# Performance work log

Hardware: AMD Instinct MI355X
Metric: run time of the kernel (lower is better)

Reference implementation:

```python
import jax, jax.numpy as jnp
import numpy as np

H = 32          # query heads
HKV = 8         # kv heads
HD = 128        # head dim
BS = 64         # sparse block size
LOCAL = 16      # local blocks
VERT = 8        # vertical stride
STEP = 1        # head sliding step = max(1, VERT // H) for non-homo heads
BASE = 1000000.0
ROPE_SCALE = 1.0
SCALE = 1.0 / np.sqrt(HD)


def setup_inputs() -> dict:
    key = jax.random.key(0)
    ks = jax.random.split(key, 6)
    T, D = 2048, H * HD
    std = 0.02
    return {
        'hidden_states': jax.random.normal(ks[0], (T, D), jnp.float32),
        'positions': jnp.arange(T, dtype=jnp.int32),
        'Wq': jax.random.normal(ks[1], (D, H * HD), jnp.float32) * std,
        'bq': jnp.zeros((H * HD,), jnp.float32),
        'Wk': jax.random.normal(ks[2], (D, HKV * HD), jnp.float32) * std,
        'bk': jnp.zeros((HKV * HD,), jnp.float32),
        'Wv': jax.random.normal(ks[3], (D, HKV * HD), jnp.float32) * std,
        'bv': jnp.zeros((HKV * HD,), jnp.float32),
        'Wo': jax.random.normal(ks[4], (D, D), jnp.float32) * std,
        'bo': jnp.zeros((D,), jnp.float32),
    }


def _rope_cos_sin(positions):
    # neox-style rotary, linear scaling (factor 1.0 -> identity)
    inv_freq = 1.0 / (BASE ** (jnp.arange(0, HD, 2, dtype=jnp.float32) / HD))  # [HD/2]
    t = positions.astype(jnp.float32) / ROPE_SCALE                             # [T]
    freqs = t[:, None] * inv_freq[None, :]                                     # [T, HD/2]
    return jnp.cos(freqs), jnp.sin(freqs)


def _apply_rope(x, cos, sin):
    # x: [T, h, HD], neox: rotate halves
    x1, x2 = x[..., : HD // 2], x[..., HD // 2 :]
    c, s = cos[:, None, :], sin[:, None, :]
    return jnp.concatenate([x1 * c - x2 * s, x2 * c + x1 * s], axis=-1)


def _block_sparse_mask(T):
    # per-head local + vertical-stride block pattern, causal at token level
    blk = jnp.arange(T) // BS
    qb, kb = blk[:, None], blk[None, :]                      # [T,T] block ids
    heads = jnp.arange(H)
    local = (qb - kb) < LOCAL                                # [T,T]
    vert = ((kb[None, :, :] + heads[:, None, None] * STEP + 1) % VERT) == 0  # [H,T,T]
    causal = jnp.arange(T)[:, None] >= jnp.arange(T)[None, :]
    return causal[None] & (local[None] | vert)               # [H,T,T] bool


def reference(hidden_states, positions, Wq, bq, Wk, bk, Wv, bv, Wo, bo):
    T = hidden_states.shape[0]
    q = (hidden_states @ Wq + bq).reshape(T, H, HD)
    k = (hidden_states @ Wk + bk).reshape(T, HKV, HD)
    v = (hidden_states @ Wv + bv).reshape(T, HKV, HD)

    cos, sin = _rope_cos_sin(positions)
    q = _apply_rope(q, cos, sin)
    k = _apply_rope(k, cos, sin)

    # GQA: repeat kv heads to match query heads
    k = jnp.repeat(k, H // HKV, axis=1)   # [T,H,HD]
    v = jnp.repeat(v, H // HKV, axis=1)

    scores = jnp.einsum('shd,thd->hst', q, k) * SCALE         # [H,T,T]
    mask = _block_sparse_mask(T)
    scores = jnp.where(mask, scores, jnp.finfo(scores.dtype).min)
    probs = jax.nn.softmax(scores, axis=-1)
    out = jnp.einsum('hst,thd->shd', probs, v).reshape(T, H * HD)
    return out @ Wo + bo
```

## Files before the change

kernel.cpp:

```cpp
#include <hip/hip_runtime.h>
#include <type_traits>

#define H_    32
#define HKV_  8
#define HD_   128
#define D_    4096
#define KVD_  1024
#define NQKV_ 6144

typedef __attribute__((ext_vector_type(8))) short s8v;
typedef __attribute__((ext_vector_type(4))) float f4v;

__device__ __forceinline__ float b2f(unsigned short u) {
  union { unsigned int i; float f; } v; v.i = ((unsigned int)u) << 16; return v.f;
}
__device__ __forceinline__ unsigned short f2b(float f) {
  unsigned int u = __float_as_uint(f);
  u += 0x7fffu + ((u >> 16) & 1u);
  return (unsigned short)(u >> 16);
}

__device__ __forceinline__ void gload16(const unsigned short* g, unsigned short* l) {
  __builtin_amdgcn_global_load_lds((const __attribute__((address_space(1))) void*)g,
                                   (__attribute__((address_space(3))) void*)l, 16, 0, 0);
}

__global__ void cvt_bf16(const float* __restrict__ x, unsigned short* __restrict__ y,
                         int n8)
{
  int i = blockIdx.x * blockDim.x + threadIdx.x;
  if (i >= n8) return;
  const float4* xp = (const float4*)x + (size_t)i * 2;
  float4 a = xp[0], b = xp[1];
  s8v v;
  v[0] = (short)f2b(a.x); v[1] = (short)f2b(a.y);
  v[2] = (short)f2b(a.z); v[3] = (short)f2b(a.w);
  v[4] = (short)f2b(b.x); v[5] = (short)f2b(b.y);
  v[6] = (short)f2b(b.z); v[7] = (short)f2b(b.w);
  *(s8v*)(y + (size_t)i * 8) = v;
}

__global__ void concat_bias(const float* __restrict__ bq, const float* __restrict__ bk,
                            const float* __restrict__ bv, float* __restrict__ o)
{
  int i = blockIdx.x * blockDim.x + threadIdx.x;
  float v = (i < D_) ? bq[i] : (i < D_ + KVD_) ? bk[i - D_] : bv[i - D_ - KVD_];
  o[i] = v;
}

__global__ __launch_bounds__(256) void cvt_transpose(
    const float* __restrict__ W, unsigned short* __restrict__ Wt, int K, int N)
{
  __shared__ unsigned short tile[64][72];
  const int k0 = blockIdx.y * 64, n0 = blockIdx.x * 64;
  const int tid = threadIdx.x;
#pragma unroll
  for (int it = 0; it < 4; ++it) {
    int idx = tid + it * 256;
    int r = idx >> 4;
    int c = (idx & 15) << 2;
    float4 w = *(const float4*)(W + (size_t)(k0 + r) * N + n0 + c);
    tile[c + 0][r] = f2b(w.x); tile[c + 1][r] = f2b(w.y);
    tile[c + 2][r] = f2b(w.z); tile[c + 3][r] = f2b(w.w);
  }
  __syncthreads();
#pragma unroll
  for (int it = 0; it < 2; ++it) {
    int idx = tid + it * 256;
    int n = idx >> 3;
    int kk = (idx & 7) << 3;
    *(s8v*)(Wt + (size_t)(n0 + n) * K + k0 + kk) = *(const s8v*)&tile[n][kk];
  }
}

__global__ __launch_bounds__(256) void vtrans(
    const unsigned short* __restrict__ S, int lds_, unsigned short* __restrict__ Dst,
    int T)
{
  __shared__ unsigned short tile[64][72];
  const int v0 = blockIdx.x * 64, t0 = blockIdx.y * 64;
  const int tid = threadIdx.x;
#pragma unroll
  for (int it = 0; it < 2; ++it) {
    int idx = tid + it * 256;
    int tr = idx >> 3;
    int vc = (idx & 7) << 3;
    s8v val = *(const s8v*)(S + (size_t)(t0 + tr) * lds_ + v0 + vc);
#pragma unroll
    for (int u = 0; u < 8; ++u) tile[vc + u][tr] = (unsigned short)val[u];
  }
  __syncthreads();
#pragma unroll
  for (int it = 0; it < 2; ++it) {
    int idx = tid + it * 256;
    int vr = idx >> 3;
    int tc = (idx & 7) << 3;
    *(s8v*)(Dst + (size_t)(v0 + vr) * T + t0 + tc) = *(const s8v*)&tile[vr][tc];
  }
}

template <typename OT>
__global__ __launch_bounds__(512, 2) void gemm_bt4p(
    const unsigned short* __restrict__ A, const unsigned short* __restrict__ Bt,
    const float* __restrict__ bias, OT* __restrict__ C,
    int M, int N, int K, int ldc)
{
  __shared__ __align__(16) unsigned short lds[65536];

  const int tid  = threadIdx.x;
  const int wave = tid >> 6;
  const int lane = tid & 63;
  const int l16  = lane & 15;
  const int quad = lane >> 4;
  const int wm   = wave >> 2;
  const int wn   = wave & 3;

  const int nbx = N >> 8;
  const int nwg = nbx * (M >> 8);
  int bid = blockIdx.x;
  if ((nwg & 7) == 0) bid = (bid & 7) * (nwg >> 3) + (bid >> 3);
  const int row0 = (bid / nbx) << 8;
  const int col0 = (bid % nbx) << 8;

  const int srow = lane >> 2;
  const int scol = (((lane & 3) ^ ((lane >> 3) & 3)) << 3);
  const unsigned short* ApL = A  + (size_t)(row0 + wave * 32 + srow) * K + scol;
  const unsigned short* BpL = Bt + (size_t)(col0 + wave * 32 + srow) * K + scol;

  unsigned short* ldsA = lds;
  unsigned short* ldsB = lds + 32768;
  const int wst = wave * 1024;

  const int sl = ((quad ^ ((l16 >> 1) & 3)) << 3);
  const int arow = wm * 128 + l16;
  const int brow = wn * 64 + l16;

  f4v acc[8][4] = {};
  const int nt = K >> 6;

  {
    const unsigned short* sa = ApL;
    const unsigned short* sb = BpL;
    gload16(sa,                       ldsA + wst);
    gload16(sa + 16 * (size_t)K,      ldsA + wst + 512);
    gload16(sb,                       ldsB + wst);
    gload16(sb + 16 * (size_t)K,      ldsB + wst + 512);
    gload16(sa + 32,                  ldsA + 8192 + wst);
    gload16(sa + 32 + 16 * (size_t)K, ldsA + 8192 + wst + 512);
    gload16(sb + 32,                  ldsB + 8192 + wst);
    gload16(sb + 32 + 16 * (size_t)K, ldsB + 8192 + wst + 512);
  }
  asm volatile("s_waitcnt vmcnt(4)" ::: "memory");
  asm volatile("s_barrier" ::: "memory");

  for (int t = 0; t < nt; ++t) {
    const int p = t & 1;
    const unsigned short* Ab0 = ldsA + p * 16384;
    const unsigned short* Ab1 = Ab0 + 8192;
    const unsigned short* Bb0 = ldsB + p * 16384;
    const unsigned short* Bb1 = Bb0 + 8192;
    unsigned short* An = ldsA + (p ^ 1) * 16384;
    unsigned short* Bn = ldsB + (p ^ 1) * 16384;
    const bool pre = (t + 1 < nt);
    const unsigned short* sa = ApL + (size_t)(t + 1) * 64;
    const unsigned short* sb = BpL + (size_t)(t + 1) * 64;

    s8v a[8], b0, b1, b2, b3;

    b0 = *(const s8v*)&Bb0[(brow +  0) * 32 + sl];
    b1 = *(const s8v*)&Bb0[(brow + 16) * 32 + sl];
#pragma unroll
    for (int i = 0; i < 8; ++i)
      a[i] = *(const s8v*)&Ab0[(arow + i * 16) * 32 + sl];
    if (pre) {
      gload16(sa,                  An + wst);
      gload16(sa + 16 * (size_t)K, An + wst + 512);
    }
    __builtin_amdgcn_s_setprio(1);
#pragma unroll
    for (int i = 0; i < 8; ++i) {
      acc[i][0] = __builtin_amdgcn_mfma_f32_16x16x32_bf16(a[i], b0, acc[i][0], 0, 0, 0);
      acc[i][1] = __builtin_amdgcn_mfma_f32_16x16x32_bf16(a[i], b1, acc[i][1], 0, 0, 0);
    }
    __builtin_amdgcn_s_setprio(0);

    b2 = *(const s8v*)&Bb0[(brow + 32) * 32 + sl];
    b3 = *(const s8v*)&Bb0[(brow + 48) * 32 + sl];
    if (pre) {
      gload16(sb,                  Bn + wst);
      gload16(sb + 16 * (size_t)K, Bn + wst + 512);
      asm volatile("s_waitcnt vmcnt(4)" ::: "memory");
    } else {
      asm volatile("s_waitcnt vmcnt(0)" ::: "memory");
    }
    asm volatile("s_barrier" ::: "memory");
    __builtin_amdgcn_s_setprio(1);
#pragma unroll
    for (int i = 0; i < 8; ++i) {
      acc[i][2] = __builtin_amdgcn_mfma_f32_16x16x32_bf16(a[i], b2, acc[i][2], 0, 0, 0);
      acc[i][3] = __builtin_amdgcn_mfma_f32_16x16x32_bf16(a[i], b3, acc[i][3], 0, 0, 0);
    }
    __builtin_amdgcn_s_setprio(0);

    b2 = *(const s8v*)&Bb1[(brow + 32) * 32 + sl];
    b3 = *(const s8v*)&Bb1[(brow + 48) * 32 + sl];
#pragma unroll
    for (int i = 0; i < 8; ++i)
      a[i] = *(const s8v*)&Ab1[(arow + i * 16) * 32 + sl];
    if (pre) {
      gload16(sa + 32,                  An + 8192 + wst);
      gload16(sa + 32 + 16 * (size_t)K, An + 8192 + wst + 512);
    }
    __builtin_amdgcn_s_setprio(1);
#pragma unroll
    for (int i = 0; i < 8; ++i) {
      acc[i][2] = __builtin_amdgcn_mfma_f32_16x16x32_bf16(a[i], b2, acc[i][2], 0, 0, 0);
      acc[i][3] = __builtin_amdgcn_mfma_f32_16x16x32_bf16(a[i], b3, acc[i][3], 0, 0, 0);
    }
    __builtin_amdgcn_s_setprio(0);

    b0 = *(const s8v*)&Bb1[(brow +  0) * 32 + sl];
    b1 = *(const s8v*)&Bb1[(brow + 16) * 32 + sl];
    if (pre) {
      gload16(sb + 32,                  Bn + 8192 + wst);
      gload16(sb + 32 + 16 * (size_t)K, Bn + 8192 + wst + 512);
      asm volatile("s_waitcnt vmcnt(4)" ::: "memory");
    }
    asm volatile("s_barrier" ::: "memory");
    __builtin_amdgcn_s_setprio(1);
#pragma unroll
    for (int i = 0; i < 8; ++i) {
      acc[i][0] = __builtin_amdgcn_mfma_f32_16x16x32_bf16(a[i], b0, acc[i][0], 0, 0, 0);
      acc[i][1] = __builtin_amdgcn_mfma_f32_16x16x32_bf16(a[i], b1, acc[i][1], 0, 0, 0);
    }
    __builtin_amdgcn_s_setprio(0);
  }

#pragma unroll
  for (int j = 0; j < 4; ++j) {
    const int col = col0 + wn * 64 + j * 16 + l16;
    const float bc = bias[col];
#pragma unroll
    for (int i = 0; i < 8; ++i) {
      const int rowb = row0 + wm * 128 + i * 16 + quad * 4;
#pragma unroll
      for (int r = 0; r < 4; ++r) {
        float o = acc[i][j][r] + bc;
        if constexpr (std::is_same_v<OT, float>) C[(size_t)(rowb + r) * ldc + col] = o;
        else                                     C[(size_t)(rowb + r) * ldc + col] = f2b(o);
      }
    }
  }
}

__global__ __launch_bounds__(256, 2) void gemm_o128(
    const unsigned short* __restrict__ A, const unsigned short* __restrict__ Bt,
    const float* __restrict__ bias, float* __restrict__ C,
    int M, int N, int K)
{
  __shared__ __align__(16) unsigned short lds[32768];

  const int tid  = threadIdx.x;
  const int wave = tid >> 6;
  const int lane = tid & 63;
  const int l16  = lane & 15;
  const int quad = lane >> 4;
  const int wm   = wave >> 1;
  const int wn   = wave & 1;

  const int nbx = N >> 7;
  const int nwg = nbx * (M >> 7);
  int bid = blockIdx.x;
  if ((nwg & 7) == 0) bid = (bid & 7) * (nwg >> 3) + (bid >> 3);
  const int row0 = (bid / nbx) << 7;
  const int col0 = (bid % nbx) << 7;

  const int srow = lane >> 2;
  const int scol = (((lane & 3) ^ ((lane >> 3) & 3)) << 3);
  const unsigned short* ApL = A  + (size_t)(row0 + wave * 16 + srow) * K + scol;
  const unsigned short* BpL = Bt + (size_t)(col0 + wave * 16 + srow) * K + scol;

  unsigned short* ldsA = lds;
  unsigned short* ldsB = lds + 16384;
  const int wst = wave * 512;

  const int sl = ((quad ^ ((l16 >> 1) & 3)) << 3);
  const int arow = wm * 64 + l16;
  const int brow = wn * 64 + l16;

  f4v acc[4][4] = {};
  const int nt = K >> 6;

  {
    const unsigned short* sa = ApL;
    const unsigned short* sb = BpL;
    gload16(sa,                       ldsA + wst);
    gload16(sa + 64 * (size_t)K,      ldsA + wst + 2048);
    gload16(sb,                       ldsB + wst);
    gload16(sb + 64 * (size_t)K,      ldsB + wst + 2048);
    gload16(sa + 32,                  ldsA + 4096 + wst);
    gload16(sa + 32 + 64 * (size_t)K, ldsA + 4096 + wst + 2048);
    gload16(sb + 32,                  ldsB + 4096 + wst);
    gload16(sb + 32 + 64 * (size_t)K, ldsB + 4096 + wst + 2048);
  }
  asm volatile("s_waitcnt vmcnt(4)" ::: "memory");
  asm volatile("s_barrier" ::: "memory");

  for (int t = 0; t < nt; ++t) {
    const int p = t & 1;
    const unsigned short* Ab0 = ldsA + p * 8192;
    const unsigned short* Ab1 = Ab0 + 4096;
    const unsigned short* Bb0 = ldsB + p * 8192;
    const unsigned short* Bb1 = Bb0 + 4096;
    unsigned short* An = ldsA + (p ^ 1) * 8192;
    unsigned short* Bn = ldsB + (p ^ 1) * 8192;
    const bool pre = (t + 1 < nt);
    const unsigned short* sa = ApL + (size_t)(t + 1) * 64;
    const unsigned short* sb = BpL + (size_t)(t + 1) * 64;

    s8v a[4], b0, b1, b2, b3;

    b0 = *(const s8v*)&Bb0[(brow +  0) * 32 + sl];
    b1 = *(const s8v*)&Bb0[(brow + 16) * 32 + sl];
#pragma unroll
    for (int i = 0; i < 4; ++i)
      a[i] = *(const s8v*)&Ab0[(arow + i * 16) * 32 + sl];
    if (pre) {
      gload16(sa,                  An + wst);
      gload16(sa + 64 * (size_t)K, An + wst + 2048);
    }
    __builtin_amdgcn_s_setprio(1);
#pragma unroll
    for (int i = 0; i < 4; ++i) {
      acc[i][0] = __builtin_amdgcn_mfma_f32_16x16x32_bf16(a[i], b0, acc[i][0], 0, 0, 0);
      acc[i][1] = __builtin_amdgcn_mfma_f32_16x16x32_bf16(a[i], b1, acc[i][1], 0, 0, 0);
    }
    __builtin_amdgcn_s_setprio(0);

    b2 = *(const s8v*)&Bb0[(brow + 32) * 32 + sl];
    b3 = *(const s8v*)&Bb0[(brow + 48) * 32 + sl];
    if (pre) {
      gload16(sb,                  Bn + wst);
      gload16(sb + 64 * (size_t)K, Bn + wst + 2048);
      asm volatile("s_waitcnt vmcnt(4)" ::: "memory");
    } else {
      asm volatile("s_waitcnt vmcnt(0)" ::: "memory");
    }
    asm volatile("s_barrier" ::: "memory");
    __builtin_amdgcn_s_setprio(1);
#pragma unroll
    for (int i = 0; i < 4; ++i) {
      acc[i][2] = __builtin_amdgcn_mfma_f32_16x16x32_bf16(a[i], b2, acc[i][2], 0, 0, 0);
      acc[i][3] = __builtin_amdgcn_mfma_f32_16x16x32_bf16(a[i], b3, acc[i][3], 0, 0, 0);
    }
    __builtin_amdgcn_s_setprio(0);

    b2 = *(const s8v*)&Bb1[(brow + 32) * 32 + sl];
    b3 = *(const s8v*)&Bb1[(brow + 48) * 32 + sl];
#pragma unroll
    for (int i = 0; i < 4; ++i)
      a[i] = *(const s8v*)&Ab1[(arow + i * 16) * 32 + sl];
    if (pre) {
      gload16(sa + 32,                  An + 4096 + wst);
      gload16(sa + 32 + 64 * (size_t)K, An + 4096 + wst + 2048);
    }
    __builtin_amdgcn_s_setprio(1);
#pragma unroll
    for (int i = 0; i < 4; ++i) {
      acc[i][2] = __builtin_amdgcn_mfma_f32_16x16x32_bf16(a[i], b2, acc[i][2], 0, 0, 0);
      acc[i][3] = __builtin_amdgcn_mfma_f32_16x16x32_bf16(a[i], b3, acc[i][3], 0, 0, 0);
    }
    __builtin_amdgcn_s_setprio(0);

    b0 = *(const s8v*)&Bb1[(brow +  0) * 32 + sl];
    b1 = *(const s8v*)&Bb1[(brow + 16) * 32 + sl];
    if (pre) {
      gload16(sb + 32,                  Bn + 4096 + wst);
      gload16(sb + 32 + 64 * (size_t)K, Bn + 4096 + wst + 2048);
      asm volatile("s_waitcnt vmcnt(4)" ::: "memory");
    }
    asm volatile("s_barrier" ::: "memory");
    __builtin_amdgcn_s_setprio(1);
#pragma unroll
    for (int i = 0; i < 4; ++i) {
      acc[i][0] = __builtin_amdgcn_mfma_f32_16x16x32_bf16(a[i], b0, acc[i][0], 0, 0, 0);
      acc[i][1] = __builtin_amdgcn_mfma_f32_16x16x32_bf16(a[i], b1, acc[i][1], 0, 0, 0);
    }
    __builtin_amdgcn_s_setprio(0);
  }

#pragma unroll
  for (int j = 0; j < 4; ++j) {
    const int col = col0 + wn * 64 + j * 16 + l16;
    const float bc = bias[col];
#pragma unroll
    for (int i = 0; i < 4; ++i) {
      const int rowb = row0 + wm * 64 + i * 16 + quad * 4;
#pragma unroll
      for (int r = 0; r < 4; ++r)
        C[(size_t)(rowb + r) * N + col] = acc[i][j][r] + bc;
    }
  }
}

__global__ void sincos_tab(const int* __restrict__ pos, float* __restrict__ ct,
                           float* __restrict__ st)
{
  const int t = blockIdx.x, d = threadIdx.x;
  float inv = powf(1.0e6f, -(float)d * (1.0f / 64.0f));
  float fr  = (float)pos[t] * inv;
  float s, c;
  sincosf(fr, &s, &c);
  ct[t * 64 + d] = c;
  st[t * 64 + d] = s;
}

__global__ void rope_apply(unsigned short* __restrict__ qkv,
                           const float* __restrict__ ct, const float* __restrict__ st,
                           int T)
{
  const int t  = blockIdx.x;
  const int hh = blockIdx.y;
  const int d  = threadIdx.x;
  unsigned short* p = qkv + (size_t)t * NQKV_ + hh * HD_;
  const float g = (hh < H_) ? (0.08838834764831845f * 1.4426950408889634f) : 1.0f;
  float c = ct[t * 64 + d], s = st[t * 64 + d];
  float x1 = b2f(p[d]), x2 = b2f(p[d + 64]);
  p[d]      = f2b((x1 * c - x2 * s) * g);
  p[d + 64] = f2b((x2 * c + x1 * s) * g);
}

__global__ __launch_bounds__(256) void attn_sparse(
    const unsigned short* __restrict__ QKV, int ldq,
    const unsigned short* __restrict__ Vt, unsigned short* __restrict__ O, int T)
{
  __shared__ __align__(16) unsigned short lds[16384];
  unsigned short* ldsK = lds;
  unsigned short* ldsV = lds + 8192;
  unsigned short* ldsP = lds;

  const int h    = blockIdx.x;
  const int qb   = (gridDim.y - 1) - blockIdx.y;
  const int hkv  = h >> 2;
  const int tid  = threadIdx.x;
  const int wave = tid >> 6;
  const int lane = tid & 63;
  const int l16  = lane & 15;
  const int quad = lane >> 4;

  const int qrow = qb * 64 + wave * 16 + l16;
  s8v qf[4];
#pragma unroll
  for (int s = 0; s < 4; ++s)
    qf[s] = *(const s8v*)(QKV + (size_t)qrow * ldq + h * HD_ + s * 32 + quad * 8);

  const int lr4 = lane >> 2;
  const int lc8 = (lane & 3) << 3;
  const unsigned short* Kp0 = QKV + (size_t)(wave * 16 + lr4) * ldq
                              + D_ + hkv * HD_ + lc8;
  unsigned short* Kd0 = ldsK + wave * 512;
  const unsigned short* Vp0 = Vt + (size_t)(hkv * HD_ + wave * 32 + lr4) * T + lc8;
  unsigned short* Vd0 = ldsV + wave * 1024;

  float mrow[4] = {-1e30f, -1e30f, -1e30f, -1e30f};
  float lrow[4] = {0.f, 0.f, 0.f, 0.f};
  f4v oacc[8] = {};
  const int rowinb = wave * 16 + quad * 4;

  for (int kb = 0; kb <= qb; ++kb) {
    if (!((qb - kb < 16) || (((kb + h + 1) & 7) == 0))) continue;

    __syncthreads();
    {
      const unsigned short* kp = Kp0 + (size_t)(kb * 64) * ldq;
      const unsigned short* vp = Vp0 + kb * 64;
#pragma unroll
      for (int t = 0; t < 4; ++t)
        gload16(kp + t * 32, Kd0 + t * 2048);
#pragma unroll
      for (int t = 0; t < 4; ++t)
        gload16(vp + (size_t)((t >> 1) * 16) * T + (t & 1) * 32,
                Vd0 + (t & 1) * 4096 + (t >> 1) * 512);
    }
    __syncthreads();

    f4v sacc[4] = {};
#pragma unroll
    for (int kt = 0; kt < 4; ++kt) {
#pragma unroll
      for (int s = 0; s < 4; ++s) {
        s8v b = *(const s8v*)&ldsK[s * 2048 + (kt * 16 + l16) * 32 + quad * 8];
        sacc[kt] = __builtin_amdgcn_mfma_f32_16x16x32_bf16(qf[s], b, sacc[kt], 0, 0, 0);
      }
    }
    __syncthreads();

    const bool diag = (kb == qb);
    float p[4][4];
#pragma unroll
    for (int r = 0; r < 4; ++r) {
      float mx = -1e30f;
#pragma unroll
      for (int kt = 0; kt < 4; ++kt) {
        float sc = sacc[kt][r];
        if (diag && (kt * 16 + l16 > rowinb + r)) sc = -1e30f;
        p[r][kt] = sc;
        mx = fmaxf(mx, sc);
      }
#pragma unroll
      for (int off = 1; off < 16; off <<= 1)
        mx = fmaxf(mx, __shfl_xor(mx, off));
      float newm = fmaxf(mrow[r], mx);
      float alpha = exp2f(mrow[r] - newm);
      mrow[r] = newm;
      float rs = 0.f;
#pragma unroll
      for (int kt = 0; kt < 4; ++kt) {
        unsigned short pb = f2b(exp2f(p[r][kt] - newm));
        ldsP[wave * 1152 + (quad * 4 + r) * 72 + kt * 16 + l16] = pb;
        rs += b2f(pb);
      }
#pragma unroll
      for (int off = 1; off < 16; off <<= 1)
        rs += __shfl_xor(rs, off);
      lrow[r] = lrow[r] * alpha + rs;
#pragma unroll
      for (int dt = 0; dt < 8; ++dt) oacc[dt][r] *= alpha;
    }

#pragma unroll
    for (int s2 = 0; s2 < 2; ++s2) {
      s8v af = *(const s8v*)&ldsP[wave * 1152 + l16 * 72 + s2 * 32 + quad * 8];
#pragma unroll
      for (int dt = 0; dt < 8; ++dt) {
        s8v vf = *(const s8v*)&ldsV[s2 * 4096 + (dt * 16 + l16) * 32 + quad * 8];
        oacc[dt] = __builtin_amdgcn_mfma_f32_16x16x32_bf16(af, vf, oacc[dt], 0, 0, 0);
      }
    }
  }

#pragma unroll
  for (int r = 0; r < 4; ++r) {
    float inv = 1.0f / lrow[r];
    size_t rowoff = (size_t)(qb * 64 + rowinb + r) * D_ + h * HD_;
#pragma unroll
    for (int dt = 0; dt < 8; ++dt)
      O[rowoff + dt * 16 + l16] = f2b(oacc[dt][r] * inv);
  }
}

extern "C" void kernel_launch(void* const* d_in, const int* in_sizes, int n_in,
                              void* d_out, int out_size, void* d_ws, size_t ws_size,
                              hipStream_t stream)
{
  const float* hs  = (const float*)d_in[0];
  const int*   pos = (const int*)d_in[1];
  const float* Wq  = (const float*)d_in[2];
  const float* bq  = (const float*)d_in[3];
  const float* Wk  = (const float*)d_in[4];
  const float* bk  = (const float*)d_in[5];
  const float* Wv  = (const float*)d_in[6];
  const float* bv  = (const float*)d_in[7];
  const float* Wo  = (const float*)d_in[8];
  const float* bo  = (const float*)d_in[9];
  float* out = (float*)d_out;

  const int T = in_sizes[1];

  const size_t nQ = (size_t)T * D_;
  unsigned short* hsb  = (unsigned short*)d_ws;
  unsigned short* qkv  = hsb + nQ;
  unsigned short* vt   = qkv + (size_t)T * NQKV_;
  unsigned short* wbuf = vt  + (size_t)KVD_ * T;
  unsigned short* tail = wbuf + (size_t)NQKV_ * D_;
  float* bqkv = (float*)tail;
  float* ct   = bqkv + NQKV_;
  float* st   = ct + (size_t)T * 64;
  unsigned short* abuf = hsb;

  dim3 blk(256);
  cvt_bf16<<<dim3((int)(nQ / 8 / 256)), blk, 0, stream>>>(hs, hsb, (int)(nQ / 8));
  concat_bias<<<dim3(NQKV_ / 256), blk, 0, stream>>>(bq, bk, bv, bqkv);
  sincos_tab<<<dim3(T), dim3(64), 0, stream>>>(pos, ct, st);

  cvt_transpose<<<dim3(D_ / 64,   D_ / 64), blk, 0, stream>>>(Wq, wbuf, D_, D_);
  cvt_transpose<<<dim3(KVD_ / 64, D_ / 64), blk, 0, stream>>>(
      Wk, wbuf + (size_t)D_ * D_, D_, KVD_);
  cvt_transpose<<<dim3(KVD_ / 64, D_ / 64), blk, 0, stream>>>(
      Wv, wbuf + (size_t)(D_ + KVD_) * D_, D_, KVD_);

  gemm_bt4p<unsigned short><<<dim3((NQKV_ / 256) * (T / 256)), dim3(512), 0, stream>>>(
      hsb, wbuf, bqkv, qkv, T, NQKV_, D_, NQKV_);

  rope_apply<<<dim3(T, H_ + HKV_), dim3(64), 0, stream>>>(qkv, ct, st, T);
  vtrans<<<dim3(KVD_ / 64, T / 64), blk, 0, stream>>>(
      qkv + D_ + KVD_, NQKV_, vt, T);

  attn_sparse<<<dim3(H_, T / 64), blk, 0, stream>>>(qkv, NQKV_, vt, abuf, T);

  cvt_transpose<<<dim3(D_ / 64, D_ / 64), blk, 0, stream>>>(Wo, wbuf, D_, D_);
  gemm_o128<<<dim3((D_ / 128) * (T / 128)), dim3(256), 0, stream>>>(
      abuf, wbuf, bo, out, T, D_, D_);
}
```

Measured before the change: 518.2 us.

## Replace output projection GEMM with 256x256 split-K kernel plus reduction

The output projection GEMM moves from 128x128 tiles with 256 threads to 256x256 tiles with 512 threads. The K dimension is split in two, so the 256 workgroups roughly match the CU count. The second K-half writes its partial sum into a scratch buffer that reuses the qkv workspace, and a separate float4 kernel adds it into the output. The goal is more reuse per tile and a grid that fills the CUs. The cost is an extra full read-modify-write pass over the 2048x4096 fp32 output, and 128KB of LDS per block, which limits occupancy.

```diff
diff --git a/kernel.cpp b/kernel.cpp
--- a/kernel.cpp
+++ b/kernel.cpp
@@ -253,85 +253,89 @@
   }
 }
 
-__global__ __launch_bounds__(256, 2) void gemm_o128(
+__global__ __launch_bounds__(512, 2) void gemm_sk(
     const unsigned short* __restrict__ A, const unsigned short* __restrict__ Bt,
-    const float* __restrict__ bias, float* __restrict__ C,
-    int M, int N, int K)
-{
-  __shared__ __align__(16) unsigned short lds[32768];
+    const float* __restrict__ bias, float* __restrict__ C0, float* __restrict__ C1,
+    int M, int N, int lda, int KS)
+{
+  __shared__ __align__(16) unsigned short lds[65536];
 
   const int tid  = threadIdx.x;
   const int wave = tid >> 6;
   const int lane = tid & 63;
   const int l16  = lane & 15;
   const int quad = lane >> 4;
-  const int wm   = wave >> 1;
-  const int wn   = wave & 1;
-
-  const int nbx = N >> 7;
-  const int nwg = nbx * (M >> 7);
+  const int wm   = wave >> 2;
+  const int wn   = wave & 3;
+
+  const int nbx   = N >> 8;
+  const int tiles = nbx * (M >> 8);
+  const int nwg   = tiles * 2;
   int bid = blockIdx.x;
   if ((nwg & 7) == 0) bid = (bid & 7) * (nwg >> 3) + (bid >> 3);
-  const int row0 = (bid / nbx) << 7;
-  const int col0 = (bid % nbx) << 7;
+  const int sid  = bid / tiles;
+  const int tb   = bid % tiles;
+  const int row0 = (tb / nbx) << 8;
+  const int col0 = (tb % nbx) << 8;
+  const int koff = sid * KS;
 
   const int srow = lane >> 2;
   const int scol = (((lane & 3) ^ ((lane >> 3) & 3)) << 3);
-  const unsigned short* ApL = A  + (size_t)(row0 + wave * 16 + srow) * K + scol;
-  const unsigned short* BpL = Bt + (size_t)(col0 + wave * 16 + srow) * K + scol;
+  const unsigned short* ApL = A  + (size_t)(row0 + wave * 32 + srow) * lda + koff + scol;
+  const unsigned short* BpL = Bt + (size_t)(col0 + wave * 32 + srow) * lda + koff + scol;
 
   unsigned short* ldsA = lds;
-  unsigned short* ldsB = lds + 16384;
-  const int wst = wave * 512;
+  unsigned short* ldsB = lds + 32768;
+  const int wst = wave * 1024;
 
   const int sl = ((quad ^ ((l16 >> 1) & 3)) << 3);
-  const int arow = wm * 64 + l16;
+  const int arow = wm * 128 + l16;
   const int brow = wn * 64 + l16;
 
-  f4v acc[4][4] = {};
-  const int nt = K >> 6;
+  f4v acc[8][4] = {};
+  const int nt = KS >> 6;
 
   {
     const unsigned short* sa = ApL;
     const unsigned short* sb = BpL;
-    gload16(sa,                       ldsA + wst);
-    gload16(sa + 64 * (size_t)K,      ldsA + wst + 2048);
-    gload16(sb,                       ldsB + wst);
-    gload16(sb + 64 * (size_t)K,      ldsB + wst + 2048);
-    gload16(sa + 32,                  ldsA + 4096 + wst);
-    gload16(sa + 32 + 64 * (size_t)K, ldsA + 4096 + wst + 2048);
-    gload16(sb + 32,                  ldsB + 4096 + wst);
-    gload16(sb + 32 + 64 * (size_t)K, ldsB + 4096 + wst + 2048);
+    gload16(sa,                         ldsA + wst);
+    gload16(sa + 16 * (size_t)lda,      ldsA + wst + 512);
+    gload16(sb,                         ldsB + wst);
+    gload16(sb + 16 * (size_t)lda,      ldsB + wst + 512);
+    gload16(sa + 32,                    ldsA + 8192 + wst);
+    gload16(sa + 32 + 16 * (size_t)lda, ldsA + 8192 + wst + 512);
+    gload16(sb + 32,                    ldsB + 8192 + wst);
+    gload16(sb + 32 + 16 * (size_t)lda, ldsB + 8192 + wst + 512);
   }
   asm volatile("s_waitcnt vmcnt(4)" ::: "memory");
   asm volatile("s_barrier" ::: "memory");
 
   for (int t = 0; t < nt; ++t) {
     const int p = t & 1;
-    const unsigned short* Ab0 = ldsA + p * 8192;
-    const unsigned short* Ab1 = Ab0 + 4096;
-    const unsigned short* Bb0 = ldsB + p * 8192;
-    const unsigned short* Bb1 = Bb0 + 4096;
-    unsigned short* An = ldsA + (p ^ 1) * 8192;
-    unsigned short* Bn = ldsB + (p ^ 1) * 8192;
+    const unsigned short* Ab0 = ldsA + p * 16384;
+    const unsigned short* Ab1 = Ab0 + 8192;
+    const unsigned short* Bb0 = ldsB + p * 16384;
+    const unsigned short* Bb1 = Bb0 + 8192;
+    unsigned short* An = ldsA + (p ^ 1) * 16384;
+    unsigned short* Bn = ldsB + (p ^ 1) * 16384;
     const bool pre = (t + 1 < nt);
     const unsigned short* sa = ApL + (size_t)(t + 1) * 64;
     const unsigned short* sb = BpL + (size_t)(t + 1) * 64;
 
-    s8v a[4], b0, b1, b2, b3;
+    s8v a[8], b0, b1, b2, b3;
 
     b0 = *(const s8v*)&Bb0[(brow +  0) * 32 + sl];
     b1 = *(const s8v*)&Bb0[(brow + 16) * 32 + sl];
 #pragma unroll
-    for (int i = 0; i < 4; ++i)
+    for (int i = 0; i < 8; ++i)
       a[i] = *(const s8v*)&Ab0[(arow + i * 16) * 32 + sl];
     if (pre) {
-      gload16(sa,                  An + wst);
-      gload16(sa + 64 * (size_t)K, An + wst + 2048);
-    }
-    __builtin_amdgcn_s_setprio(1);
-#pragma unroll
-    for (int i = 0; i < 4; ++i) {
+      gload16(sa,                    An + wst);
+      gload16(sa + 16 * (size_t)lda, An + wst + 512);
+    }
+    __builtin_amdgcn_s_setprio(1);
+#pragma unroll
+    for (int i = 0; i < 8; ++i) {
       acc[i][0] = __builtin_amdgcn_mfma_f32_16x16x32_bf16(a[i], b0, acc[i][0], 0, 0, 0);
       acc[i][1] = __builtin_amdgcn_mfma_f32_16x16x32_bf16(a[i], b1, acc[i][1], 0, 0, 0);
     }
@@ -340,8 +344,8 @@
     b2 = *(const s8v*)&Bb0[(brow + 32) * 32 + sl];
     b3 = *(const s8v*)&Bb0[(brow + 48) * 32 + sl];
     if (pre) {
-      gload16(sb,                  Bn + wst);
-      gload16(sb + 64 * (size_t)K, Bn + wst + 2048);
+      gload16(sb,                    Bn + wst);
+      gload16(sb + 16 * (size_t)lda, Bn + wst + 512);
       asm volatile("s_waitcnt vmcnt(4)" ::: "memory");
     } else {
       asm volatile("s_waitcnt vmcnt(0)" ::: "memory");
@@ -349,7 +353,7 @@
     asm volatile("s_barrier" ::: "memory");
     __builtin_amdgcn_s_setprio(1);
 #pragma unroll
-    for (int i = 0; i < 4; ++i) {
+    for (int i = 0; i < 8; ++i) {
       acc[i][2] = __builtin_amdgcn_mfma_f32_16x16x32_bf16(a[i], b2, acc[i][2], 0, 0, 0);
       acc[i][3] = __builtin_amdgcn_mfma_f32_16x16x32_bf16(a[i], b3, acc[i][3], 0, 0, 0);
     }
@@ -358,15 +362,15 @@
     b2 = *(const s8v*)&Bb1[(brow + 32) * 32 + sl];
     b3 = *(const s8v*)&Bb1[(brow + 48) * 32 + sl];
 #pragma unroll
-    for (int i = 0; i < 4; ++i)
+    for (int i = 0; i < 8; ++i)
       a[i] = *(const s8v*)&Ab1[(arow + i * 16) * 32 + sl];
     if (pre) {
-      gload16(sa + 32,                  An + 4096 + wst);
-      gload16(sa + 32 + 64 * (size_t)K, An + 4096 + wst + 2048);
-    }
-    __builtin_amdgcn_s_setprio(1);
-#pragma unroll
-    for (int i = 0; i < 4; ++i) {
+      gload16(sa + 32,                    An + 8192 + wst);
+      gload16(sa + 32 + 16 * (size_t)lda, An + 8192 + wst + 512);
+    }
+    __builtin_amdgcn_s_setprio(1);
+#pragma unroll
+    for (int i = 0; i < 8; ++i) {
       acc[i][2] = __builtin_amdgcn_mfma_f32_16x16x32_bf16(a[i], b2, acc[i][2], 0, 0, 0);
       acc[i][3] = __builtin_amdgcn_mfma_f32_16x16x32_bf16(a[i], b3, acc[i][3], 0, 0, 0);
     }
@@ -375,31 +379,45 @@
     b0 = *(const s8v*)&Bb1[(brow +  0) * 32 + sl];
     b1 = *(const s8v*)&Bb1[(brow + 16) * 32 + sl];
     if (pre) {
-      gload16(sb + 32,                  Bn + 4096 + wst);
-      gload16(sb + 32 + 64 * (size_t)K, Bn + 4096 + wst + 2048);
+      gload16(sb + 32,                    Bn + 8192 + wst);
+      gload16(sb + 32 + 16 * (size_t)lda, Bn + 8192 + wst + 512);
       asm volatile("s_waitcnt vmcnt(4)" ::: "memory");
     }
     asm volatile("s_barrier" ::: "memory");
     __builtin_amdgcn_s_setprio(1);
 #pragma unroll
-    for (int i = 0; i < 4; ++i) {
+    for (int i = 0; i < 8; ++i) {
       acc[i][0] = __builtin_amdgcn_mfma_f32_16x16x32_bf16(a[i], b0, acc[i][0], 0, 0, 0);
       acc[i][1] = __builtin_amdgcn_mfma_f32_16x16x32_bf16(a[i], b1, acc[i][1], 0, 0, 0);
     }
     __builtin_amdgcn_s_setprio(0);
   }
 
+  float* Cw = sid ? C1 : C0;
 #pragma unroll
   for (int j = 0; j < 4; ++j) {
     const int col = col0 + wn * 64 + j * 16 + l16;
-    const float bc = bias[col];
-#pragma unroll
-    for (int i = 0; i < 4; ++i) {
-      const int rowb = row0 + wm * 64 + i * 16 + quad * 4;
+    const float bc = sid ? 0.0f : bias[col];
+#pragma unroll
+    for (int i = 0; i < 8; ++i) {
+      const int rowb = row0 + wm * 128 + i * 16 + quad * 4;
 #pragma unroll
       for (int r = 0; r < 4; ++r)
-        C[(size_t)(rowb + r) * N + col] = acc[i][j][r] + bc;
-    }
+        Cw[(size_t)(rowb + r) * N + col] = acc[i][j][r] + bc;
+    }
+  }
+}
+
+__global__ __launch_bounds__(256) void reduce_add(
+    float* __restrict__ out, const float* __restrict__ c1, int n4)
+{
+  int i = blockIdx.x * blockDim.x + threadIdx.x;
+  const int stride = gridDim.x * blockDim.x;
+  for (; i < n4; i += stride) {
+    float4 a = ((const float4*)out)[i];
+    float4 b = ((const float4*)c1)[i];
+    a.x += b.x; a.y += b.y; a.z += b.z; a.w += b.w;
+    ((float4*)out)[i] = a;
   }
 }
 
@@ -578,6 +596,9 @@
   float* st   = ct + (size_t)T * 64;
   unsigned short* abuf = hsb;
 
+  unsigned short* woT = wbuf + 8388608;
+  float* c1 = (float*)qkv;
+
   dim3 blk(256);
   cvt_bf16<<<dim3((int)(nQ / 8 / 256)), blk, 0, stream>>>(hs, hsb, (int)(nQ / 8));
   concat_bias<<<dim3(NQKV_ / 256), blk, 0, stream>>>(bq, bk, bv, bqkv);
@@ -598,7 +619,8 @@
 
   attn_sparse<<<dim3(H_, T / 64), blk, 0, stream>>>(qkv, NQKV_, vt, abuf, T);
 
-  cvt_transpose<<<dim3(D_ / 64, D_ / 64), blk, 0, stream>>>(Wo, wbuf, D_, D_);
-  gemm_o128<<<dim3((D_ / 128) * (T / 128)), dim3(256), 0, stream>>>(
-      abuf, wbuf, bo, out, T, D_, D_);
-}
+  cvt_transpose<<<dim3(D_ / 64, D_ / 64), blk, 0, stream>>>(Wo, woT, D_, D_);
+  gemm_sk<<<dim3(2 * (D_ / 256) * (T / 256)), dim3(512), 0, stream>>>(
+      abuf, woT, bo, out, c1, T, D_, D_, D_ / 2);
+  reduce_add<<<dim3(2048), blk, 0, stream>>>(out, c1, (int)(nQ / 4));
+}
```

After: 509.8 us. About the same (-1.6%).
